# Optimization experiments

Hardware: AMD Instinct MI355X
Metric: run time of the kernel (lower is better)

## Reference

```python
import jax, jax.numpy as jnp
import numpy as np

NUM_GENES = 20000
NUM_CLASS = 32
BATCH_SIZE = 8
N = NUM_GENES * BATCH_SIZE      # 160_000 total nodes
E = 2_560_000                    # edges (avg degree 16)
K = 10
ALPHA = 0.1


def setup_inputs() -> dict:
    key = jax.random.key(0)
    ks = jax.random.split(key, 9)
    x = jax.random.normal(ks[0], (N, 1), dtype=jnp.float32)
    edge_index = jax.random.randint(ks[1], (2, E), 0, N, dtype=jnp.int32)
    batch = jnp.repeat(jnp.arange(BATCH_SIZE, dtype=jnp.int32), NUM_GENES)
    exp_emb_table = jax.random.normal(ks[2], (NUM_GENES, NUM_CLASS), dtype=jnp.float32) * 0.1
    exp_bias_table = jax.random.normal(ks[3], (NUM_GENES, 1), dtype=jnp.float32) * 0.1
    s = 1.0 / np.sqrt(NUM_CLASS)
    W1 = jax.random.uniform(ks[4], (NUM_CLASS, NUM_CLASS), jnp.float32, -s, s)
    b1 = jax.random.uniform(ks[5], (NUM_CLASS,), jnp.float32, -s, s)
    W2 = jax.random.uniform(ks[6], (NUM_CLASS, NUM_CLASS), jnp.float32, -s, s)
    b2 = jax.random.uniform(ks[7], (NUM_CLASS,), jnp.float32, -s, s)
    return {"x": x, "edge_index": edge_index, "batch": batch,
            "exp_emb_table": exp_emb_table, "exp_bias_table": exp_bias_table,
            "W1": W1, "b1": b1, "W2": W2, "b2": b2}


def reference(x, edge_index, batch, exp_emb_table, exp_bias_table, W1, b1, W2, b2):
    # node_index tiles 0..num_genes-1 for each graph in the batch
    node_index = jnp.tile(jnp.arange(NUM_GENES), BATCH_SIZE)        # [N]
    h = exp_emb_table[node_index] * x + exp_bias_table[node_index]  # [N, C]
    # dropout is identity in eval mode
    h = jax.nn.relu(h @ W1.T + b1)
    h = h @ W2.T + b2

    # APPNP: gcn_norm with self-loops, then k power-iteration steps
    loops = jnp.arange(N, dtype=edge_index.dtype)
    row = jnp.concatenate([edge_index[0], loops])  # source
    col = jnp.concatenate([edge_index[1], loops])  # target
    deg = jax.ops.segment_sum(jnp.ones_like(col, dtype=h.dtype), col, num_segments=N)
    dinv = jnp.where(deg > 0, jax.lax.rsqrt(deg), 0.0)
    norm = (dinv[row] * dinv[col])[:, None]        # [E+N, 1]

    h0 = h
    def step(carry, _):
        agg = jax.ops.segment_sum(carry[row] * norm, col, num_segments=N)
        return (1.0 - ALPHA) * agg + ALPHA * h0, None
    h, _ = jax.lax.scan(step, h, None, length=K)

    # global mean pool over graphs
    sums = jax.ops.segment_sum(h, batch, num_segments=BATCH_SIZE)
    counts = jax.ops.segment_sum(jnp.ones((N, 1), h.dtype), batch, num_segments=BATCH_SIZE)
    return sums / counts  # [BATCH_SIZE, NUM_CLASS]
```

## Files before the change

kernel.cpp:

```cpp
#include <hip/hip_runtime.h>

typedef unsigned int u32;
typedef unsigned short u16;

#define NPB 64
#define P1CHUNK 8192
#define DPCHUNK 8192
#define SPB 16
#define DHCHUNK 8
#define OUT_CHUNK 640

__device__ inline float bf2f(u16 b) { return __uint_as_float(((u32)b) << 16); }
__device__ inline u16 f2bf(float f) {
    u32 u = __float_as_uint(f);
    return (u16)((u + 0x7fffu + ((u >> 16) & 1u)) >> 16);
}
__device__ inline u32 pack2(float a, float b) { return (u32)f2bf(a) | ((u32)f2bf(b) << 16); }

__global__ void k_zero_i(int* __restrict__ p, int n) {
    int i = blockIdx.x * 256 + threadIdx.x;
    if (i < n) p[i] = 0;
}

__global__ void k_cnt(const int* __restrict__ ei, int E,
                      int* __restrict__ bcnt, int* __restrict__ dscnt, int nbuckets) {
    extern __shared__ int h[];
    for (int i = threadIdx.x; i < nbuckets + 64; i += blockDim.x) h[i] = 0;
    __syncthreads();
    int stride = gridDim.x * blockDim.x;
    for (int e = blockIdx.x * blockDim.x + threadIdx.x; e < E; e += stride) {
        atomicAdd(&h[ei[e] >> 6], 1);
        atomicAdd(&h[nbuckets + (ei[E + e] >> 12)], 1);
    }
    __syncthreads();
    for (int i = threadIdx.x; i < nbuckets; i += blockDim.x) {
        int v = h[i];
        if (v) atomicAdd(&bcnt[i], v);
    }
    if (threadIdx.x < 64) {
        int v = h[nbuckets + threadIdx.x];
        if (v) atomicAdd(&dscnt[threadIdx.x], v);
    }
}

__global__ void k_scanB(const int* __restrict__ bcnt, int nbuckets,
                        const int* __restrict__ dscnt,
                        int* __restrict__ boff, int* __restrict__ bCur,
                        int* __restrict__ soff, int* __restrict__ sCur,
                        int* __restrict__ dsoff, int* __restrict__ dsCur,
                        int* __restrict__ offsets, int N, int E, int nsup, int nsupD) {
    __shared__ int s[1024];
    __shared__ int carry;
    int t = threadIdx.x;
    if (t == 0) carry = 0;
    __syncthreads();
    for (int base = 0; base < nbuckets; base += 1024) {
        int i = base + t;
        int v = (i < nbuckets) ? bcnt[i] : 0;
        s[t] = v;
        __syncthreads();
        for (int off = 1; off < 1024; off <<= 1) {
            int tmp = (t >= off) ? s[t - off] : 0;
            __syncthreads();
            s[t] += tmp;
            __syncthreads();
        }
        int pos = s[t] - v + carry;
        if (i < nbuckets) {
            boff[i] = pos;
            bCur[i] = pos;
            if ((i & 63) == 0) { soff[i >> 6] = pos; sCur[i >> 6] = pos; }
        }
        __syncthreads();
        if (t == 1023) carry += s[1023];
        __syncthreads();
    }
    if (t == 0) {
        boff[nbuckets] = E; soff[nsup] = E; offsets[N] = E;
        int acc = 0;
        for (int i = 0; i < nsupD; ++i) {
            dsoff[i] = acc; dsCur[i] = acc;
            acc += dscnt[i];
        }
        dsoff[nsupD] = E;
    }
}

__global__ __launch_bounds__(512) void k_p1(const int* __restrict__ ei, int E,
                                            int* __restrict__ sCur, u32* __restrict__ buf1) {
    __shared__ int cnt[64];
    __shared__ int cur[64];
    int c0 = blockIdx.x * P1CHUNK;
    int c1 = min(E, c0 + P1CHUNK);
    int t = threadIdx.x;
    if (t < 64) cnt[t] = 0;
    __syncthreads();
    for (int e = c0 + t; e < c1; e += 512)
        atomicAdd(&cnt[ei[e] >> 12], 1);
    __syncthreads();
    if (t < 64) {
        int c = cnt[t];
        cur[t] = (c > 0) ? atomicAdd(&sCur[t], c) : 0;
    }
    __syncthreads();
    for (int e = c0 + t; e < c1; e += 512) {
        int s = ei[e];
        int d = ei[E + e];
        int p = atomicAdd(&cur[s >> 12], 1);
        buf1[p] = (u32)(d & 0x3FFFF) | ((u32)(s & 4095) << 18);
    }
}

__global__ __launch_bounds__(256) void k_dp1(const int* __restrict__ col, int E,
                                             int* __restrict__ dsCur, u16* __restrict__ dbuf) {
    __shared__ int cnt[64];
    __shared__ int cur[64];
    int c0 = blockIdx.x * DPCHUNK;
    int c1 = min(E, c0 + DPCHUNK);
    int t = threadIdx.x;
    if (t < 64) cnt[t] = 0;
    __syncthreads();
    for (int e = c0 + t; e < c1; e += 256)
        atomicAdd(&cnt[col[e] >> 12], 1);
    __syncthreads();
    if (t < 64) {
        int c = cnt[t];
        cur[t] = (c > 0) ? atomicAdd(&dsCur[t], c) : 0;
    }
    __syncthreads();
    for (int e = c0 + t; e < c1; e += 256) {
        int d = col[e];
        int p = atomicAdd(&cur[d >> 12], 1);
        dbuf[p] = (u16)(d & 4095);
    }
}

__global__ __launch_bounds__(256) void k_dhist(const u16* __restrict__ dbuf,
                                               const int* __restrict__ dsoff,
                                               int* __restrict__ deg, int N) {
    __shared__ int h[4096];
    int sup = blockIdx.x / DHCHUNK;
    int ch = blockIdx.x % DHCHUNK;
    int t = threadIdx.x;
    for (int i = t; i < 4096; i += 256) h[i] = 0;
    __syncthreads();
    int s0 = dsoff[sup], s1 = dsoff[sup + 1];
    int per = (s1 - s0 + DHCHUNK - 1) / DHCHUNK;
    int c0 = s0 + ch * per;
    int c1 = min(s1, c0 + per);
    for (int e = c0 + t; e < c1; e += 256)
        atomicAdd(&h[dbuf[e]], 1);
    __syncthreads();
    int vbase = sup << 12;
    for (int i = t; i < 4096; i += 256) {
        int v = h[i];
        if (v && vbase + i < N) atomicAdd(&deg[vbase + i], v);
    }
}

__global__ __launch_bounds__(256) void k_p2(const u32* __restrict__ buf1,
                                            const int* __restrict__ soff,
                                            int* __restrict__ bCur,
                                            u32* __restrict__ binned) {
    __shared__ int cnt[64];
    __shared__ int cur[64];
    int sb = blockIdx.x / SPB;
    int ch = blockIdx.x % SPB;
    int s0 = soff[sb], s1 = soff[sb + 1];
    int per = (s1 - s0 + SPB - 1) / SPB;
    int c0 = s0 + ch * per;
    int c1 = min(s1, c0 + per);
    int t = threadIdx.x;
    if (t < 64) cnt[t] = 0;
    __syncthreads();
    for (int e = c0 + t; e < c1; e += 256)
        atomicAdd(&cnt[(buf1[e] >> 24) & 63], 1);
    __syncthreads();
    if (t < 64) {
        int c = cnt[t];
        cur[t] = (c > 0) ? atomicAdd(&bCur[(sb << 6) + t], c) : 0;
    }
    __syncthreads();
    for (int e = c0 + t; e < c1; e += 256) {
        u32 v = buf1[e];
        int p = atomicAdd(&cur[(v >> 24) & 63], 1);
        binned[p] = v & 0x00FFFFFFu;
    }
}

__global__ __launch_bounds__(256) void k_sort(const u32* __restrict__ binned,
                                              const int* __restrict__ boff,
                                              int* __restrict__ offsets,
                                              int* __restrict__ dsts, int N) {
    __shared__ int cnt[64];
    __shared__ int off[64];
    int b = blockIdx.x;
    int s0 = boff[b], s1 = boff[b + 1];
    int t = threadIdx.x;
    if (t < 64) cnt[t] = 0;
    __syncthreads();
    for (int e = s0 + t; e < s1; e += 256)
        atomicAdd(&cnt[(binned[e] >> 18) & 63], 1);
    __syncthreads();
    if (t == 0) {
        int acc = s0;
        #pragma unroll
        for (int i = 0; i < 64; ++i) { off[i] = acc; acc += cnt[i]; }
    }
    __syncthreads();
    int vbase = b << 6;
    if (t < 64 && vbase + t < N) offsets[vbase + t] = off[t];
    __syncthreads();
    if (t < 64) cnt[t] = off[t];
    __syncthreads();
    for (int e = s0 + t; e < s1; e += 256) {
        u32 v = binned[e];
        int p = atomicAdd(&cnt[(v >> 18) & 63], 1);
        dsts[p] = (int)(v & 0x3FFFFu);
    }
}

__global__ void k_dinv(const int* __restrict__ deg, float* __restrict__ dinv,
                       float* __restrict__ a, float* __restrict__ rd, int N) {
    int i = blockIdx.x * 256 + threadIdx.x;
    if (i < N) {
        float d = (float)(deg[i] + 1);
        float dv = rsqrtf(d);
        dinv[i] = dv;
        a[i] = 0.9f * dv * dv;
        rd[i] = sqrtf(d);
    }
}

__global__ __launch_bounds__(256) void k_AW(const float* __restrict__ emb,
                                            const float* __restrict__ W1,
                                            float* __restrict__ A, int ngenes) {
    __shared__ float w1[32][33];
    __shared__ float eb[8][33];
    int t = threadIdx.x;
    int j = t & 31, gl = t >> 5;
    for (int i = t; i < 1024; i += 256) w1[i >> 5][i & 31] = W1[i];
    int g = blockIdx.x * 8 + gl;
    if (g < ngenes) eb[gl][j] = emb[g * 32 + j];
    __syncthreads();
    if (g < ngenes) {
        float acc = 0.f;
        #pragma unroll
        for (int c = 0; c < 32; ++c) acc = fmaf(eb[gl][c], w1[j][c], acc);
        A[(size_t)g * 32 + j] = acc;
    }
}

__global__ void k_s1(const float* __restrict__ W1, float* __restrict__ s1) {
    int j = threadIdx.x;
    if (j < 32) {
        float acc = 0.f;
        #pragma unroll
        for (int c = 0; c < 32; ++c) acc += W1[j * 32 + c];
        s1[j] = acc;
    }
}

__global__ __launch_bounds__(256) void k_h0(const float* __restrict__ x,
                                            const float* __restrict__ A,
                                            const float* __restrict__ bias,
                                            const float* __restrict__ s1,
                                            const float* __restrict__ b1,
                                            const float* __restrict__ W2,
                                            const float* __restrict__ b2,
                                            const float* __restrict__ dinv,
                                            uint4* __restrict__ h0,
                                            uint4* __restrict__ q0,
                                            float* __restrict__ out, int out_n,
                                            int N, int ngenes) {
    int node = blockIdx.x * 256 + threadIdx.x;
    if (blockIdx.x == 0 && threadIdx.x < out_n) out[threadIdx.x] = 0.f;
    if (node >= N) return;
    int g = node % ngenes;
    float xv = x[node];
    float bv = bias[g];
    const float4* Ar = (const float4*)(A + (size_t)g * 32);
    float r1[32];
    #pragma unroll
    for (int q = 0; q < 8; ++q) {
        float4 a4 = Ar[q];
        r1[q * 4 + 0] = fmaxf(fmaf(xv, a4.x, fmaf(bv, s1[q * 4 + 0], b1[q * 4 + 0])), 0.f);
        r1[q * 4 + 1] = fmaxf(fmaf(xv, a4.y, fmaf(bv, s1[q * 4 + 1], b1[q * 4 + 1])), 0.f);
        r1[q * 4 + 2] = fmaxf(fmaf(xv, a4.z, fmaf(bv, s1[q * 4 + 2], b1[q * 4 + 2])), 0.f);
        r1[q * 4 + 3] = fmaxf(fmaf(xv, a4.w, fmaf(bv, s1[q * 4 + 3], b1[q * 4 + 3])), 0.f);
    }
    u32 ow[16];
    #pragma unroll
    for (int i = 0; i < 32; i += 2) {
        float accA = b2[i];
        float accB = b2[i + 1];
        #pragma unroll
        for (int j2 = 0; j2 < 32; ++j2) {
            accA = fmaf(r1[j2], W2[i * 32 + j2], accA);
            accB = fmaf(r1[j2], W2[(i + 1) * 32 + j2], accB);
        }
        ow[i >> 1] = pack2(accA, accB);
    }
    #pragma unroll
    for (int q = 0; q < 4; ++q) {
        uint4 o;
        o.x = ow[q * 4 + 0];
        o.y = ow[q * 4 + 1];
        o.z = ow[q * 4 + 2];
        o.w = ow[q * 4 + 3];
        h0[(size_t)node * 4 + q] = o;
    }
    int gb = node / ngenes;
    u32 lo = (u32)f2bf(dinv[node]);
    u32 hi = lo << 16;
    uint4 qo;
    qo.x = (gb == 0) ? lo : (gb == 1) ? hi : 0u;
    qo.y = (gb == 2) ? lo : (gb == 3) ? hi : 0u;
    qo.z = (gb == 4) ? lo : (gb == 5) ? hi : 0u;
    qo.w = (gb == 6) ? lo : (gb == 7) ? hi : 0u;
    q0[node] = qo;
}

__global__ __launch_bounds__(256) void k_prop8(const uint4* __restrict__ qin,
                                               uint4* __restrict__ qout,
                                               const float* __restrict__ a,
                                               const float* __restrict__ dinv,
                                               const int* __restrict__ offsets,
                                               const int* __restrict__ dsts,
                                               int N, int ngenes) {
    int node = blockIdx.x * 256 + threadIdx.x;
    if (node >= N) return;
    int s0 = offsets[node];
    int s1 = offsets[node + 1];
    uint4 self = qin[node];
    float c0 = bf2f((u16)self.x), c1 = bf2f((u16)(self.x >> 16));
    float c2 = bf2f((u16)self.y), c3 = bf2f((u16)(self.y >> 16));
    float c4 = bf2f((u16)self.z), c5 = bf2f((u16)(self.z >> 16));
    float c6 = bf2f((u16)self.w), c7 = bf2f((u16)(self.w >> 16));
    int e = s0;
    for (; e + 4 <= s1; e += 4) {
        uint4 vA = qin[dsts[e]];
        uint4 vB = qin[dsts[e + 1]];
        uint4 vC = qin[dsts[e + 2]];
        uint4 vD = qin[dsts[e + 3]];
        c0 += bf2f((u16)vA.x) + bf2f((u16)vB.x) + bf2f((u16)vC.x) + bf2f((u16)vD.x);
        c1 += bf2f((u16)(vA.x >> 16)) + bf2f((u16)(vB.x >> 16)) + bf2f((u16)(vC.x >> 16)) + bf2f((u16)(vD.x >> 16));
        c2 += bf2f((u16)vA.y) + bf2f((u16)vB.y) + bf2f((u16)vC.y) + bf2f((u16)vD.y);
        c3 += bf2f((u16)(vA.y >> 16)) + bf2f((u16)(vB.y >> 16)) + bf2f((u16)(vC.y >> 16)) + bf2f((u16)(vD.y >> 16));
        c4 += bf2f((u16)vA.z) + bf2f((u16)vB.z) + bf2f((u16)vC.z) + bf2f((u16)vD.z);
        c5 += bf2f((u16)(vA.z >> 16)) + bf2f((u16)(vB.z >> 16)) + bf2f((u16)(vC.z >> 16)) + bf2f((u16)(vD.z >> 16));
        c6 += bf2f((u16)vA.w) + bf2f((u16)vB.w) + bf2f((u16)vC.w) + bf2f((u16)vD.w);
        c7 += bf2f((u16)(vA.w >> 16)) + bf2f((u16)(vB.w >> 16)) + bf2f((u16)(vC.w >> 16)) + bf2f((u16)(vD.w >> 16));
    }
    for (; e < s1; ++e) {
        uint4 v = qin[dsts[e]];
        c0 += bf2f((u16)v.x); c1 += bf2f((u16)(v.x >> 16));
        c2 += bf2f((u16)v.y); c3 += bf2f((u16)(v.y >> 16));
        c4 += bf2f((u16)v.z); c5 += bf2f((u16)(v.z >> 16));
        c6 += bf2f((u16)v.w); c7 += bf2f((u16)(v.w >> 16));
    }
    float av = a[node];
    float qi = 0.1f * dinv[node];
    int gb = node / ngenes;
    c0 = av * c0 + ((gb == 0) ? qi : 0.f);
    c1 = av * c1 + ((gb == 1) ? qi : 0.f);
    c2 = av * c2 + ((gb == 2) ? qi : 0.f);
    c3 = av * c3 + ((gb == 3) ? qi : 0.f);
    c4 = av * c4 + ((gb == 4) ? qi : 0.f);
    c5 = av * c5 + ((gb == 5) ? qi : 0.f);
    c6 = av * c6 + ((gb == 6) ? qi : 0.f);
    c7 = av * c7 + ((gb == 7) ? qi : 0.f);
    uint4 o;
    o.x = pack2(c0, c1);
    o.y = pack2(c2, c3);
    o.z = pack2(c4, c5);
    o.w = pack2(c6, c7);
    qout[node] = o;
}

__global__ __launch_bounds__(256) void k_out(const uint4* __restrict__ q,
                                             const u16* __restrict__ h0,
                                             const float* __restrict__ rd,
                                             float* __restrict__ out,
                                             int N, int ngenes) {
    __shared__ float wq[64][8];
    __shared__ u16 hs[64][32];
    int t = threadIdx.x;
    int b = t >> 5, c = t & 31;
    float acc = 0.f;
    int base = blockIdx.x * OUT_CHUNK;
    int lim = min(N, base + OUT_CHUNK);
    for (int v0 = base; v0 < lim; v0 += 64) {
        int nv = min(64, lim - v0);
        __syncthreads();
        int r = t >> 2, w4 = t & 3;
        if (r < nv) {
            *(uint4*)&hs[r][w4 * 8] = ((const uint4*)(h0 + (size_t)(v0 + r) * 32))[w4];
            u32 wv = ((const u32*)&q[v0 + r])[w4];
            float rdv = rd[v0 + r];
            wq[r][w4 * 2] = bf2f((u16)wv) * rdv;
            wq[r][w4 * 2 + 1] = bf2f((u16)(wv >> 16)) * rdv;
        }
        __syncthreads();
        for (int i = 0; i < nv; ++i)
            acc = fmaf(wq[i][b], bf2f(hs[i][c]), acc);
    }
    atomicAdd(&out[b * 32 + c], acc / (float)ngenes);
}

extern "C" void kernel_launch(void* const* d_in, const int* in_sizes, int n_in,
                              void* d_out, int out_size, void* d_ws, size_t ws_size,
                              hipStream_t stream) {
    const float* x    = (const float*)d_in[0];
    const int*   ei   = (const int*)d_in[1];
    const float* emb  = (const float*)d_in[3];
    const float* bias = (const float*)d_in[4];
    const float* W1   = (const float*)d_in[5];
    const float* b1   = (const float*)d_in[6];
    const float* W2   = (const float*)d_in[7];
    const float* b2   = (const float*)d_in[8];
    float* out = (float*)d_out;

    int N = in_sizes[0];
    int E = in_sizes[1] / 2;
    int ngenes = in_sizes[4];
    int nbuckets = (N + NPB - 1) / NPB;
    int nsup = (nbuckets + 63) / 64;
    int nsupD = (N + 4095) / 4096;

    char* pws = (char*)d_ws;
    auto carve = [&](size_t bytes) {
        void* r = (void*)pws;
        pws += (bytes + 255) & ~(size_t)255;
        return r;
    };
    u16*   h0      = (u16*)carve((size_t)N * 32 * 2);
    uint4* qA      = (uint4*)carve((size_t)N * 16);
    uint4* qB      = (uint4*)carve((size_t)N * 16);
    float* Amat    = (float*)carve((size_t)ngenes * 32 * 4);
    float* s1v     = (float*)carve(32 * 4);
    float* dinv    = (float*)carve((size_t)N * 4);
    float* afac    = (float*)carve((size_t)N * 4);
    float* rd      = (float*)carve((size_t)N * 4);
    int*   offsets = (int*)carve((size_t)(N + 1) * 4);
    int*   deg     = (int*)carve((size_t)N * 4);
    int*   bcnt    = (int*)carve((size_t)nbuckets * 4);
    int*   dscnt   = (int*)carve(64 * 4);
    int*   boff    = (int*)carve((size_t)(nbuckets + 1) * 4);
    int*   bCur    = (int*)carve((size_t)nbuckets * 4);
    int*   soff    = (int*)carve(65 * 4);
    int*   sCur    = (int*)carve(64 * 4);
    int*   dsoff   = (int*)carve(65 * 4);
    int*   dsCur   = (int*)carve(64 * 4);
    u32*   buf1    = (u32*)carve((size_t)E * 4);
    u32*   binned  = (u32*)carve((size_t)E * 4);
    int*   dsts    = (int*)carve((size_t)E * 4);
    u16*   dbuf    = (u16*)carve((size_t)E * 2);

    int nbN = (N + 255) / 256;
    int zlen = (int)(dscnt - deg) + 64;

    hipLaunchKernelGGL(k_zero_i, dim3((zlen + 255) / 256), dim3(256), 0, stream, deg, zlen);
    hipLaunchKernelGGL(k_cnt, dim3(160), dim3(256), (nbuckets + 64) * 4, stream,
                       ei, E, bcnt, dscnt, nbuckets);
    hipLaunchKernelGGL(k_scanB, dim3(1), dim3(1024), 0, stream,
                       bcnt, nbuckets, dscnt, boff, bCur, soff, sCur, dsoff, dsCur,
                       offsets, N, E, nsup, nsupD);
    hipLaunchKernelGGL(k_p1, dim3((E + P1CHUNK - 1) / P1CHUNK), dim3(512), 0, stream,
                       ei, E, sCur, buf1);
    hipLaunchKernelGGL(k_dp1, dim3((E + DPCHUNK - 1) / DPCHUNK), dim3(256), 0, stream,
                       ei + E, E, dsCur, dbuf);
    hipLaunchKernelGGL(k_dhist, dim3(nsupD * DHCHUNK), dim3(256), 0, stream,
                       dbuf, dsoff, deg, N);
    hipLaunchKernelGGL(k_dinv, dim3(nbN), dim3(256), 0, stream, deg, dinv, afac, rd, N);
    hipLaunchKernelGGL(k_p2, dim3(nsup * SPB), dim3(256), 0, stream, buf1, soff, bCur, binned);
    hipLaunchKernelGGL(k_sort, dim3(nbuckets), dim3(256), 0, stream,
                       binned, boff, offsets, dsts, N);
    hipLaunchKernelGGL(k_AW, dim3((ngenes + 7) / 8), dim3(256), 0, stream, emb, W1, Amat, ngenes);
    hipLaunchKernelGGL(k_s1, dim3(1), dim3(64), 0, stream, W1, s1v);
    hipLaunchKernelGGL(k_h0, dim3(nbN), dim3(256), 0, stream,
                       x, Amat, bias, s1v, b1, W2, b2, dinv,
                       (uint4*)h0, qA, out, out_size, N, ngenes);

    const uint4* qin = qA;
    for (int it = 0; it < 10; ++it) {
        uint4* qo = (it & 1) ? qA : qB;
        hipLaunchKernelGGL(k_prop8, dim3(nbN), dim3(256), 0, stream,
                           qin, qo, afac, dinv, offsets, dsts, N, ngenes);
        qin = qo;
    }

    hipLaunchKernelGGL(k_out, dim3((N + OUT_CHUNK - 1) / OUT_CHUNK), dim3(256), 0, stream,
                       qin, h0, rd, out, N, ngenes);
}
```

Before: 386.0 us.

## Split bucket counting into per-block partials with merge, fuse partition passes

The counting kernel now runs on many more blocks and writes per-block histograms to a workspace buffer. A separate merge kernel reduces them with few global atomics, replacing the atomic flush at the end of each block. The two partition kernels, by source and by destination, are fused into one pass over the edge list with smaller chunks, so the destination array is read once less. In exchange it adds a large partial-count buffer (CNTB*M ints), one extra kernel launch, and a more scattered write pattern per block in the fused partition.

```diff
diff --git a/kernel.cpp b/kernel.cpp
--- a/kernel.cpp
+++ b/kernel.cpp
@@ -4,8 +4,9 @@
 typedef unsigned short u16;
 
 #define NPB 64
-#define P1CHUNK 8192
-#define DPCHUNK 8192
+#define CNTB 768
+#define MSEG 4
+#define PCHUNK 4096
 #define SPB 16
 #define DHCHUNK 8
 #define OUT_CHUNK 640
@@ -23,23 +24,33 @@
 }
 
 __global__ void k_cnt(const int* __restrict__ ei, int E,
-                      int* __restrict__ bcnt, int* __restrict__ dscnt, int nbuckets) {
+                      int* __restrict__ pcnt, int nbuckets) {
     extern __shared__ int h[];
-    for (int i = threadIdx.x; i < nbuckets + 64; i += blockDim.x) h[i] = 0;
-    __syncthreads();
-    int stride = gridDim.x * blockDim.x;
-    for (int e = blockIdx.x * blockDim.x + threadIdx.x; e < E; e += stride) {
+    int M = nbuckets + 64;
+    for (int i = threadIdx.x; i < M; i += 256) h[i] = 0;
+    __syncthreads();
+    int stride = gridDim.x * 256;
+    for (int e = blockIdx.x * 256 + threadIdx.x; e < E; e += stride) {
         atomicAdd(&h[ei[e] >> 6], 1);
         atomicAdd(&h[nbuckets + (ei[E + e] >> 12)], 1);
     }
     __syncthreads();
-    for (int i = threadIdx.x; i < nbuckets; i += blockDim.x) {
-        int v = h[i];
-        if (v) atomicAdd(&bcnt[i], v);
-    }
-    if (threadIdx.x < 64) {
-        int v = h[nbuckets + threadIdx.x];
-        if (v) atomicAdd(&dscnt[threadIdx.x], v);
+    int* dst = pcnt + (size_t)blockIdx.x * M;
+    for (int i = threadIdx.x; i < M; i += 256) dst[i] = h[i];
+}
+
+__global__ void k_merge(const int* __restrict__ pcnt, int M, int nbuckets,
+                        int* __restrict__ bcnt, int* __restrict__ dscnt) {
+    int bin = blockIdx.x * 256 + threadIdx.x;
+    if (bin >= M) return;
+    int per = (CNTB + MSEG - 1) / MSEG;
+    int b0 = blockIdx.y * per;
+    int b1 = min(CNTB, b0 + per);
+    int s = 0;
+    for (int b = b0; b < b1; ++b) s += pcnt[(size_t)b * M + bin];
+    if (s) {
+        if (bin < nbuckets) atomicAdd(&bcnt[bin], s);
+        else atomicAdd(&dscnt[bin - nbuckets], s);
     }
 }
 
@@ -86,21 +97,28 @@
     }
 }
 
-__global__ __launch_bounds__(512) void k_p1(const int* __restrict__ ei, int E,
-                                            int* __restrict__ sCur, u32* __restrict__ buf1) {
+__global__ __launch_bounds__(512) void k_part(const int* __restrict__ ei, int E,
+                                              int* __restrict__ sCur, int* __restrict__ dsCur,
+                                              u32* __restrict__ buf1, u16* __restrict__ dbuf) {
     __shared__ int cnt[64];
     __shared__ int cur[64];
-    int c0 = blockIdx.x * P1CHUNK;
-    int c1 = min(E, c0 + P1CHUNK);
-    int t = threadIdx.x;
-    if (t < 64) cnt[t] = 0;
-    __syncthreads();
-    for (int e = c0 + t; e < c1; e += 512)
+    __shared__ int dcnt[64];
+    __shared__ int dcur[64];
+    int c0 = blockIdx.x * PCHUNK;
+    int c1 = min(E, c0 + PCHUNK);
+    int t = threadIdx.x;
+    if (t < 64) { cnt[t] = 0; dcnt[t] = 0; }
+    __syncthreads();
+    for (int e = c0 + t; e < c1; e += 512) {
         atomicAdd(&cnt[ei[e] >> 12], 1);
+        atomicAdd(&dcnt[ei[E + e] >> 12], 1);
+    }
     __syncthreads();
     if (t < 64) {
         int c = cnt[t];
-        cur[t] = (c > 0) ? atomicAdd(&sCur[t], c) : 0;
+        cur[t] = c ? atomicAdd(&sCur[t], c) : 0;
+        int dc = dcnt[t];
+        dcur[t] = dc ? atomicAdd(&dsCur[t], dc) : 0;
     }
     __syncthreads();
     for (int e = c0 + t; e < c1; e += 512) {
@@ -108,30 +126,8 @@
         int d = ei[E + e];
         int p = atomicAdd(&cur[s >> 12], 1);
         buf1[p] = (u32)(d & 0x3FFFF) | ((u32)(s & 4095) << 18);
-    }
-}
-
-__global__ __launch_bounds__(256) void k_dp1(const int* __restrict__ col, int E,
-                                             int* __restrict__ dsCur, u16* __restrict__ dbuf) {
-    __shared__ int cnt[64];
-    __shared__ int cur[64];
-    int c0 = blockIdx.x * DPCHUNK;
-    int c1 = min(E, c0 + DPCHUNK);
-    int t = threadIdx.x;
-    if (t < 64) cnt[t] = 0;
-    __syncthreads();
-    for (int e = c0 + t; e < c1; e += 256)
-        atomicAdd(&cnt[col[e] >> 12], 1);
-    __syncthreads();
-    if (t < 64) {
-        int c = cnt[t];
-        cur[t] = (c > 0) ? atomicAdd(&dsCur[t], c) : 0;
-    }
-    __syncthreads();
-    for (int e = c0 + t; e < c1; e += 256) {
-        int d = col[e];
-        int p = atomicAdd(&cur[d >> 12], 1);
-        dbuf[p] = (u16)(d & 4095);
+        int pd = atomicAdd(&dcur[d >> 12], 1);
+        dbuf[pd] = (u16)(d & 4095);
     }
 }
 
@@ -427,6 +423,7 @@
     int nbuckets = (N + NPB - 1) / NPB;
     int nsup = (nbuckets + 63) / 64;
     int nsupD = (N + 4095) / 4096;
+    int M = nbuckets + 64;
 
     char* pws = (char*)d_ws;
     auto carve = [&](size_t bytes) {
@@ -452,6 +449,7 @@
     int*   sCur    = (int*)carve(64 * 4);
     int*   dsoff   = (int*)carve(65 * 4);
     int*   dsCur   = (int*)carve(64 * 4);
+    int*   pcnt    = (int*)carve((size_t)CNTB * M * 4);
     u32*   buf1    = (u32*)carve((size_t)E * 4);
     u32*   binned  = (u32*)carve((size_t)E * 4);
     int*   dsts    = (int*)carve((size_t)E * 4);
@@ -461,15 +459,14 @@
     int zlen = (int)(dscnt - deg) + 64;
 
     hipLaunchKernelGGL(k_zero_i, dim3((zlen + 255) / 256), dim3(256), 0, stream, deg, zlen);
-    hipLaunchKernelGGL(k_cnt, dim3(160), dim3(256), (nbuckets + 64) * 4, stream,
-                       ei, E, bcnt, dscnt, nbuckets);
+    hipLaunchKernelGGL(k_cnt, dim3(CNTB), dim3(256), M * 4, stream, ei, E, pcnt, nbuckets);
+    hipLaunchKernelGGL(k_merge, dim3((M + 255) / 256, MSEG), dim3(256), 0, stream,
+                       pcnt, M, nbuckets, bcnt, dscnt);
     hipLaunchKernelGGL(k_scanB, dim3(1), dim3(1024), 0, stream,
                        bcnt, nbuckets, dscnt, boff, bCur, soff, sCur, dsoff, dsCur,
                        offsets, N, E, nsup, nsupD);
-    hipLaunchKernelGGL(k_p1, dim3((E + P1CHUNK - 1) / P1CHUNK), dim3(512), 0, stream,
-                       ei, E, sCur, buf1);
-    hipLaunchKernelGGL(k_dp1, dim3((E + DPCHUNK - 1) / DPCHUNK), dim3(256), 0, stream,
-                       ei + E, E, dsCur, dbuf);
+    hipLaunchKernelGGL(k_part, dim3((E + PCHUNK - 1) / PCHUNK), dim3(512), 0, stream,
+                       ei, E, sCur, dsCur, buf1, dbuf);
     hipLaunchKernelGGL(k_dhist, dim3(nsupD * DHCHUNK), dim3(256), 0, stream,
                        dbuf, dsoff, deg, N);
     hipLaunchKernelGGL(k_dinv, dim3(nbN), dim3(256), 0, stream, deg, dinv, afac, rd, N);
```

Measured after the change: 398.4 us. 1.03x slower.
